# Kernel optimization log

Hardware: AMD Instinct MI355X
Metric: run time of the kernel (lower is better)

## Reference

```python
import jax, jax.numpy as jnp
import numpy as np

B, T, D, H, O = 128, 512, 512, 1024, 256
FORGET_BIAS = 1.0


def setup_inputs() -> dict:
    key = jax.random.key(0)
    ks = jax.random.split(key, 4)
    inputs = jax.random.normal(ks[0], (B * T, D), dtype=jnp.float32)
    # padded sequence lengths; ensure max == T so the reshape to [B, T, D] is exact
    seq_lens = jax.random.randint(ks[1], (B,), T // 2, T + 1, dtype=jnp.int32).at[0].set(T)
    c_in = jnp.zeros((B, H), jnp.float32)
    h_in = jnp.zeros((B, H), jnp.float32)
    W_lstm = jax.random.normal(ks[2], (D + H, 4 * H), dtype=jnp.float32) * (1.0 / np.sqrt(D + H))
    b_lstm = jnp.zeros((4 * H,), jnp.float32)
    W_out = jax.random.normal(ks[3], (H, O), dtype=jnp.float32) * 0.01  # normc_initializer(0.01)-scale
    b_out = jnp.zeros((O,), jnp.float32)
    return {"inputs": inputs, "c_in": c_in, "h_in": h_in, "W_lstm": W_lstm,
            "b_lstm": b_lstm, "W_out": W_out, "b_out": b_out, "seq_lens": seq_lens}


def reference(inputs, c_in, h_in, W_lstm, b_lstm, W_out, b_out, seq_lens):
    # add_time_dimension: [B*T, D] -> [B, T, D]; scan is time-major -> [T, B, D]
    xs = inputs.reshape(B, T, D).transpose(1, 0, 2)
    ts = jnp.arange(T, dtype=seq_lens.dtype)

    def step(carry, inp):
        c, h = carry
        x_t, t = inp
        gates = jnp.concatenate([x_t, h], axis=-1) @ W_lstm + b_lstm  # [B, 4H]
        i, j, f, o = jnp.split(gates, 4, axis=-1)  # BasicLSTMCell gate order
        new_c = c * jax.nn.sigmoid(f + FORGET_BIAS) + jax.nn.sigmoid(i) * jnp.tanh(j)
        new_h = jnp.tanh(new_c) * jax.nn.sigmoid(o)
        valid = (t < seq_lens)[:, None]  # dynamic_rnn sequence_length semantics
        c2 = jnp.where(valid, new_c, c)
        h2 = jnp.where(valid, new_h, h)
        out = jnp.where(valid, new_h, 0.0)  # outputs zeroed past seq_len
        return (c2, h2), out

    (c_out, h_out), outs = jax.lax.scan(step, (c_in, h_in), (xs, ts))
    lstm_out = outs.transpose(1, 0, 2).reshape(-1, H)  # [B*T, H]
    logits = lstm_out @ W_out + b_out  # [B*T, O]
    return logits, lstm_out, c_out, h_out
```

## Files before the change

### kernel.cpp

```cpp
#include <hip/hip_runtime.h>


typedef _Float16 f16;
typedef _Float16 half8 __attribute__((ext_vector_type(8)));
typedef float floatx4 __attribute__((ext_vector_type(4)));

#define AS1 __attribute__((address_space(1)))
#define AS3 __attribute__((address_space(3)))

__device__ __forceinline__ void gload_lds16(const void* g, void* l) {
  __builtin_amdgcn_global_load_lds((const AS1 void*)g, (AS3 void*)l, 16, 0, 0);
}
__device__ __forceinline__ void gload_lds16_coh(const void* g, void* l) {
  __builtin_amdgcn_global_load_lds((const AS1 void*)g, (AS3 void*)l, 16, 0, 17);
}

__device__ __forceinline__ int load_flag_coh(const int* p) {
  int v;
  asm volatile("global_load_dword %0, %1, off sc0 sc1\n\ts_waitcnt vmcnt(0)"
               : "=v"(v) : "v"(p) : "memory");
  return v;
}
__device__ __forceinline__ void store_flag_coh(int* p, int v) {
  asm volatile("global_store_dword %0, %1, off sc0 sc1" :: "v"(p), "v"(v) : "memory");
}
__device__ __forceinline__ void store_h_coh(f16* p, f16 v) {
  unsigned int uv = (unsigned int)__builtin_bit_cast(unsigned short, v);
  asm volatile("global_store_short %0, %1, off sc0 sc1" :: "v"(p), "v"(uv) : "memory");
}

__device__ __forceinline__ float sigm(float x) { return 1.f / (1.f + __expf(-x)); }
__device__ __forceinline__ float tanh_fast(float x) {
  float ax = fabsf(x);
  float e = __expf(2.f * ax);
  float t = 1.f - 2.f / (e + 1.f);
  return copysignf(t, x);
}

static constexpr size_t XW_OFF  = 0;
static constexpr size_t XW_BY   = (size_t)65536 * 4096 * 2;
static constexpr size_t L16_OFF = XW_OFF + XW_BY;
static constexpr size_t L16_BY  = (size_t)65536 * 1024 * 2;
static constexpr size_t IN16_OFF = L16_OFF;
static constexpr size_t WXT_OFF = L16_OFF + L16_BY;
static constexpr size_t WXT_BY  = (size_t)4096 * 512 * 2;
static constexpr size_t WOT_OFF = WXT_OFF + WXT_BY;
static constexpr size_t WOT_BY  = (size_t)256 * 1024 * 2;
static constexpr size_t WPK_OFF = WOT_OFF + WOT_BY;
static constexpr size_t WPK_BY  = (size_t)524288 * 8 * 2;
static constexpr size_t TH_OFF  = WPK_OFF + WPK_BY;
static constexpr size_t TH_BY   = (size_t)2 * 128 * 1024 * 2;
static constexpr size_t FLG_OFF = TH_OFF + TH_BY;
static constexpr size_t FLG_BY  = (size_t)8 * 32 * 4;
static constexpr size_t WS_NEED = FLG_OFF + FLG_BY;

__global__ __launch_bounds__(256) void conv_f32_to_f16(const float* __restrict__ in,
                                                       f16* __restrict__ out) {
  size_t i = (size_t)blockIdx.x * 256 + threadIdx.x;
  const float4* in4 = (const float4*)in;
  float4 a = in4[i * 2], b = in4[i * 2 + 1];
  half8 v = {(f16)a.x, (f16)a.y, (f16)a.z, (f16)a.w,
             (f16)b.x, (f16)b.y, (f16)b.z, (f16)b.w};
  *(half8*)(out + i * 8) = v;
}

__global__ __launch_bounds__(256) void transpose_f32_to_f16(const float* __restrict__ in,
                                                            f16* __restrict__ out,
                                                            int R, int C) {
  __shared__ float tile[64][65];
  int tx = threadIdx.x & 63, ty = threadIdx.x >> 6;
  int c0 = blockIdx.x * 64, r0 = blockIdx.y * 64;
#pragma unroll
  for (int q = 0; q < 16; ++q) {
    int r = q * 4 + ty;
    tile[r][tx] = in[(size_t)(r0 + r) * C + c0 + tx];
  }
  __syncthreads();
#pragma unroll
  for (int q = 0; q < 16; ++q) {
    int oc = q * 4 + ty;
    out[(size_t)(c0 + oc) * R + r0 + tx] = (f16)tile[tx][oc];
  }
}

__global__ __launch_bounds__(256) void pack_wh(const float* __restrict__ W,
                                               f16* __restrict__ wpack) {
  int s = blockIdx.x * 256 + threadIdx.x;
  int lane = s & 63;
  int ks = (s >> 6) & 7;
  int ni = (s >> 9) & 3;
  int w  = (s >> 11) & 7;
  int cb = s >> 14;
  int nh = w & 1, ksl = w >> 1;
  int c = nh * 64 + ni * 16 + (lane & 15);
  int g = c >> 5, ul = c & 31;
  int ncol = g * 1024 + cb * 32 + ul;
  int kb = ksl * 256 + ks * 32 + (lane >> 4) * 8;
  half8 v;
#pragma unroll
  for (int e = 0; e < 8; ++e)
    v[e] = (f16)W[(size_t)(512 + kb + e) * 4096 + ncol];
  ((half8*)wpack)[s] = v;
}

template <typename OT>
__global__ __launch_bounds__(256) void gemm_f16(const f16* __restrict__ A,
                                                const f16* __restrict__ Bt,
                                                const float* __restrict__ bias,
                                                OT* __restrict__ C,
                                                int M, int N, int K) {
  __shared__ __align__(16) char smem[32768];
  const int tid = threadIdx.x;
  const int n0 = blockIdx.x * 128, m0 = blockIdx.y * 128;
  const int l = tid & 63, w = tid >> 6;
  const int wr = w >> 1, wc = w & 1;
  const int r16 = l & 15, hi = l >> 4;
  floatx4 acc[4][4];
#pragma unroll
  for (int a = 0; a < 4; ++a)
#pragma unroll
    for (int b = 0; b < 4; ++b) acc[a][b] = (floatx4){0.f, 0.f, 0.f, 0.f};

  const int nk = K >> 6;
  for (int kk = 0; kk < nk; ++kk) {
    __syncthreads();
#pragma unroll
    for (int q = 0; q < 4; ++q) {
      int c = q * 256 + tid;
      int row = c >> 3, g8 = c & 7;
      gload_lds16(A + (size_t)(m0 + row) * K + kk * 64 + g8 * 8, smem + c * 16);
    }
#pragma unroll
    for (int q = 0; q < 4; ++q) {
      int c = q * 256 + tid;
      int row = c >> 3, g8 = c & 7;
      gload_lds16(Bt + (size_t)(n0 + row) * K + kk * 64 + g8 * 8, smem + 16384 + c * 16);
    }
    __syncthreads();
#pragma unroll
    for (int ks = 0; ks < 2; ++ks) {
      half8 af[4], bf[4];
#pragma unroll
      for (int mi = 0; mi < 4; ++mi)
        af[mi] = *(const half8*)(smem + ((wr * 64 + mi * 16 + r16) * 64 + ks * 32 + hi * 8) * 2);
#pragma unroll
      for (int ni = 0; ni < 4; ++ni)
        bf[ni] = *(const half8*)(smem + 16384 +
                                 ((wc * 64 + ni * 16 + r16) * 64 + ks * 32 + hi * 8) * 2);
#pragma unroll
      for (int mi = 0; mi < 4; ++mi)
#pragma unroll
        for (int ni = 0; ni < 4; ++ni)
          acc[mi][ni] = __builtin_amdgcn_mfma_f32_16x16x32_f16(af[mi], bf[ni], acc[mi][ni], 0, 0, 0);
    }
  }
#pragma unroll
  for (int ni = 0; ni < 4; ++ni) {
    int col = n0 + wc * 64 + ni * 16 + r16;
    float bv = bias[col];
#pragma unroll
    for (int mi = 0; mi < 4; ++mi)
#pragma unroll
      for (int rr = 0; rr < 4; ++rr) {
        int row = m0 + wr * 64 + mi * 16 + hi * 4 + rr;
        C[(size_t)row * N + col] = (OT)(acc[mi][ni][rr] + bv);
      }
  }
}

__global__ __launch_bounds__(512, 2)
void lstm_phase2(const f16* __restrict__ wpack, const f16* __restrict__ xw,
                 const float* __restrict__ c_in, const float* __restrict__ h_in,
                 const int* __restrict__ seq_lens,
                 f16* teamh, int* flags,
                 float* __restrict__ lstm_out, f16* __restrict__ lstm16,
                 float* __restrict__ c_out, float* __restrict__ h_out) {
  __shared__ __align__(16) char smem[65536];
  const int tid = threadIdx.x;
  const int bk = blockIdx.x;
  const int team = bk >> 5, cb = bk & 31;
  const int b0 = team * 16;
  const int u0 = cb * 32;
  const int l = tid & 63, w = tid >> 6;
  const int nh = w & 1, ksl = w >> 1;
  const int r16 = l & 15, hi = l >> 4;

  half8 wf[4][8];
  {
    const half8* wp = (const half8*)wpack;
    size_t base = (size_t)((cb * 8 + w) * 4) * 8 * 64;
#pragma unroll
    for (int ni = 0; ni < 4; ++ni)
#pragma unroll
      for (int ks = 0; ks < 8; ++ks)
        wf[ni][ks] = wp[base + (size_t)(ni * 8 + ks) * 64 + l];
  }

  const int bb = tid >> 5, ul = tid & 31;
  const int bglob = b0 + bb;
  const int nunit = u0 + ul;
  float creg = c_in[bglob * 1024 + nunit];
  float hreg = h_in[bglob * 1024 + nunit];
  const int slen = seq_lens[bglob];

  float* red = (float*)(smem + 32768);
  int* myflags = flags + team * 32;

#pragma unroll 1
  for (int t = 0; t < 512; ++t) {
    f16 xwv0, xwv1, xwv2, xwv3;
    {
      const f16* xp = xw + ((size_t)bglob * 512 + t) * 4096 + nunit;
      xwv0 = xp[0]; xwv1 = xp[1024]; xwv2 = xp[2048]; xwv3 = xp[3072];
    }

    if (t > 0) {
      if (tid < 64) {
        const int* fp = myflags + (tid & 31);
        while (true) {
          int g = load_flag_coh(fp);
          if (__all((tid >= 32) | (g >= t))) break;
          __builtin_amdgcn_s_sleep(1);
        }
      }
      __syncthreads();
      const char* hb = (const char*)teamh + (size_t)(t & 1) * (128 * 1024 * 2);
#pragma unroll
      for (int q = 0; q < 4; ++q) {
        int G = q * 512 + tid;
        int r = G >> 7, p = G & 127;
        int dg = p ^ (r & 7);
        gload_lds16_coh(hb + ((size_t)(b0 + r) * 1024 + dg * 8) * 2, smem + G * 16);
      }
    } else {
#pragma unroll
      for (int q = 0; q < 4; ++q) {
        int G = q * 512 + tid;
        int r = G >> 7, p = G & 127;
        int dg = p ^ (r & 7);
        const float* s = h_in + (size_t)(b0 + r) * 1024 + dg * 8;
        half8 v;
#pragma unroll
        for (int e = 0; e < 8; ++e) v[e] = (f16)s[e];
        *(half8*)(smem + G * 16) = v;
      }
    }
    __syncthreads();

    floatx4 acc0 = {0.f, 0.f, 0.f, 0.f}, acc1 = acc0, acc2 = acc0, acc3 = acc0;
#pragma unroll
    for (int ks = 0; ks < 8; ++ks) {
      int gran = ksl * 32 + ks * 4 + hi;
      int phys = gran ^ (r16 & 7);
      half8 a = *(const half8*)(smem + r16 * 2048 + phys * 16);
      acc0 = __builtin_amdgcn_mfma_f32_16x16x32_f16(a, wf[0][ks], acc0, 0, 0, 0);
      acc1 = __builtin_amdgcn_mfma_f32_16x16x32_f16(a, wf[1][ks], acc1, 0, 0, 0);
      acc2 = __builtin_amdgcn_mfma_f32_16x16x32_f16(a, wf[2][ks], acc2, 0, 0, 0);
      acc3 = __builtin_amdgcn_mfma_f32_16x16x32_f16(a, wf[3][ks], acc3, 0, 0, 0);
    }
    {
      int cbase = nh * 64 + r16;
      int rbase = ksl * 16 + hi * 4;
#pragma unroll
      for (int rr = 0; rr < 4; ++rr) {
        float* rp = red + (size_t)(rbase + rr) * 128 + cbase;
        rp[0] = acc0[rr]; rp[16] = acc1[rr]; rp[32] = acc2[rr]; rp[48] = acc3[rr];
      }
    }
    __syncthreads();

    float g0 = (float)xwv0, g1 = (float)xwv1, g2 = (float)xwv2, g3 = (float)xwv3;
#pragma unroll
    for (int p = 0; p < 4; ++p) {
      const float* rp = red + ((size_t)p * 16 + bb) * 128 + ul;
      g0 += rp[0]; g1 += rp[32]; g2 += rp[64]; g3 += rp[96];
    }
    float nc = creg * sigm(g2 + 1.f) + sigm(g0) * tanh_fast(g1);
    float nhv = tanh_fast(nc) * sigm(g3);
    bool valid = t < slen;
    if (valid) { creg = nc; hreg = nhv; }
    float outv = valid ? nhv : 0.f;
    size_t orow = ((size_t)bglob * 512 + t) * 1024 + nunit;

    store_h_coh(teamh + (size_t)((t + 1) & 1) * 131072 + bglob * 1024 + nunit, (f16)hreg);
    lstm_out[orow] = outv;
    lstm16[orow] = (f16)outv;

    asm volatile("s_waitcnt vmcnt(0)" ::: "memory");
    __syncthreads();
    if (tid == 0) store_flag_coh(myflags + cb, t + 1);
  }

  c_out[bglob * 1024 + nunit] = creg;
  h_out[bglob * 1024 + nunit] = hreg;
}

extern "C" void kernel_launch(void* const* d_in, const int* in_sizes, int n_in,
                              void* d_out, int out_size, void* d_ws, size_t ws_size,
                              hipStream_t stream) {
  const float* inputs  = (const float*)d_in[0];
  const float* c_in    = (const float*)d_in[1];
  const float* h_in    = (const float*)d_in[2];
  const float* W_lstm  = (const float*)d_in[3];
  const float* b_lstm  = (const float*)d_in[4];
  const float* W_out   = (const float*)d_in[5];
  const float* b_out   = (const float*)d_in[6];
  const int*   seq_lens= (const int*)d_in[7];

  float* logits  = (float*)d_out;
  float* lstm_out= logits + (size_t)65536 * 256;
  float* c_out   = lstm_out + (size_t)65536 * 1024;
  float* h_out   = c_out + (size_t)128 * 1024;

  if (ws_size < WS_NEED) return;

  char* ws = (char*)d_ws;
  f16* xw    = (f16*)(ws + XW_OFF);
  f16* in16  = (f16*)(ws + IN16_OFF);
  f16* l16   = (f16*)(ws + L16_OFF);
  f16* wxt   = (f16*)(ws + WXT_OFF);
  f16* wot   = (f16*)(ws + WOT_OFF);
  f16* wpk   = (f16*)(ws + WPK_OFF);
  f16* teamh = (f16*)(ws + TH_OFF);
  int* flags = (int*)(ws + FLG_OFF);

  hipMemsetAsync(flags, 0, FLG_BY, stream);
  conv_f32_to_f16<<<16384, 256, 0, stream>>>(inputs, in16);
  transpose_f32_to_f16<<<dim3(64, 8), 256, 0, stream>>>(W_lstm, wxt, 512, 4096);
  transpose_f32_to_f16<<<dim3(4, 16), 256, 0, stream>>>(W_out, wot, 1024, 256);
  pack_wh<<<2048, 256, 0, stream>>>(W_lstm, wpk);

  gemm_f16<f16><<<dim3(32, 512), 256, 0, stream>>>(in16, wxt, b_lstm, xw, 65536, 4096, 512);

  {
    const f16* wpk_c = wpk;
    const f16* xw_c  = xw;
    void* args[] = {(void*)&wpk_c, (void*)&xw_c, (void*)&c_in, (void*)&h_in,
                    (void*)&seq_lens, (void*)&teamh, (void*)&flags,
                    (void*)&lstm_out, (void*)&l16, (void*)&c_out, (void*)&h_out};
    hipLaunchCooperativeKernel((void*)lstm_phase2, dim3(256), dim3(512), args, 0, stream);
  }

  gemm_f16<float><<<dim3(2, 512), 256, 0, stream>>>(l16, wot, b_out, logits, 65536, 256, 1024);
}
```

Baseline: 2.379 ms.

## Replace per-block flag barrier with per-wave atomic counters and per-wave h loads

Each wave now atomically increments its block's step counter right after storing its h values. Consumer waves poll only the 8 producer blocks covering their K-slice and load just that slice of h directly into LDS. This removes the block-wide syncthreads and single-thread flag store from the critical step-to-step path. The LDS layout for h is reorganized per K-slice, and the reduction buffer gets an XOR swizzle to avoid bank conflicts. The costs are more atomic traffic and polling, plus subtler memory-ordering assumptions.

```diff
diff --git a/kernel.cpp b/kernel.cpp
--- a/kernel.cpp
+++ b/kernel.cpp
@@ -15,14 +15,11 @@
   __builtin_amdgcn_global_load_lds((const AS1 void*)g, (AS3 void*)l, 16, 0, 17);
 }
 
-__device__ __forceinline__ int load_flag_coh(const int* p) {
+__device__ __forceinline__ int load_flag_coh(const unsigned* p) {
   int v;
   asm volatile("global_load_dword %0, %1, off sc0 sc1\n\ts_waitcnt vmcnt(0)"
                : "=v"(v) : "v"(p) : "memory");
   return v;
-}
-__device__ __forceinline__ void store_flag_coh(int* p, int v) {
-  asm volatile("global_store_dword %0, %1, off sc0 sc1" :: "v"(p), "v"(v) : "memory");
 }
 __device__ __forceinline__ void store_h_coh(f16* p, f16 v) {
   unsigned int uv = (unsigned int)__builtin_bit_cast(unsigned short, v);
@@ -172,7 +169,7 @@
 void lstm_phase2(const f16* __restrict__ wpack, const f16* __restrict__ xw,
                  const float* __restrict__ c_in, const float* __restrict__ h_in,
                  const int* __restrict__ seq_lens,
-                 f16* teamh, int* flags,
+                 f16* teamh, unsigned* flags,
                  float* __restrict__ lstm_out, f16* __restrict__ lstm16,
                  float* __restrict__ c_out, float* __restrict__ h_out) {
   __shared__ __align__(16) char smem[65536];
@@ -204,7 +201,8 @@
   const int slen = seq_lens[bglob];
 
   float* red = (float*)(smem + 32768);
-  int* myflags = flags + team * 32;
+  unsigned* myflag = flags + team * 32 + cb;
+  const unsigned* pollf = flags + team * 32 + ksl * 8 + (l & 7);
 
 #pragma unroll 1
   for (int t = 0; t < 512; ++t) {
@@ -215,34 +213,33 @@
     }
 
     if (t > 0) {
-      if (tid < 64) {
-        const int* fp = myflags + (tid & 31);
-        while (true) {
-          int g = load_flag_coh(fp);
-          if (__all((tid >= 32) | (g >= t))) break;
-          __builtin_amdgcn_s_sleep(1);
-        }
-      }
-      __syncthreads();
-      const char* hb = (const char*)teamh + (size_t)(t & 1) * (128 * 1024 * 2);
-#pragma unroll
-      for (int q = 0; q < 4; ++q) {
-        int G = q * 512 + tid;
-        int r = G >> 7, p = G & 127;
-        int dg = p ^ (r & 7);
-        gload_lds16_coh(hb + ((size_t)(b0 + r) * 1024 + dg * 8) * 2, smem + G * 16);
-      }
+      const int tgt = 8 * t;
+      while (true) {
+        int g = load_flag_coh(pollf);
+        if (__all((l >= 8) || (g >= tgt))) break;
+        __builtin_amdgcn_s_sleep(1);
+      }
+      asm volatile("" ::: "memory");
+      const char* hb = (const char*)teamh + (size_t)(t & 1) * (131072 * 2);
+#pragma unroll
+      for (int j = 0; j < 4; ++j) {
+        int rj = nh * 8 + 2 * j + (l >> 5);
+        int ql = (l & 31) ^ (rj & 7);
+        gload_lds16_coh(hb + ((size_t)(b0 + rj) * 1024 + ksl * 256 + ql * 8) * 2,
+                        smem + (ksl * 512 + (nh * 8 + 2 * j) * 32) * 16);
+      }
+      asm volatile("s_waitcnt vmcnt(0)" ::: "memory");
     } else {
 #pragma unroll
-      for (int q = 0; q < 4; ++q) {
-        int G = q * 512 + tid;
-        int r = G >> 7, p = G & 127;
-        int dg = p ^ (r & 7);
-        const float* s = h_in + (size_t)(b0 + r) * 1024 + dg * 8;
+      for (int j = 0; j < 4; ++j) {
+        int idx = j * 512 + tid;
+        int ks_s = idx >> 9, rem = idx & 511, r = rem >> 5, qs = rem & 31;
+        int ql = qs ^ (r & 7);
+        const float* s = h_in + (size_t)(b0 + r) * 1024 + ks_s * 256 + ql * 8;
         half8 v;
 #pragma unroll
         for (int e = 0; e < 8; ++e) v[e] = (f16)s[e];
-        *(half8*)(smem + G * 16) = v;
+        *(half8*)(smem + idx * 16) = v;
       }
     }
     __syncthreads();
@@ -250,9 +247,8 @@
     floatx4 acc0 = {0.f, 0.f, 0.f, 0.f}, acc1 = acc0, acc2 = acc0, acc3 = acc0;
 #pragma unroll
     for (int ks = 0; ks < 8; ++ks) {
-      int gran = ksl * 32 + ks * 4 + hi;
-      int phys = gran ^ (r16 & 7);
-      half8 a = *(const half8*)(smem + r16 * 2048 + phys * 16);
+      int pq = (ks * 4 + hi) ^ (r16 & 7);
+      half8 a = *(const half8*)(smem + ksl * 8192 + r16 * 512 + pq * 16);
       acc0 = __builtin_amdgcn_mfma_f32_16x16x32_f16(a, wf[0][ks], acc0, 0, 0, 0);
       acc1 = __builtin_amdgcn_mfma_f32_16x16x32_f16(a, wf[1][ks], acc1, 0, 0, 0);
       acc2 = __builtin_amdgcn_mfma_f32_16x16x32_f16(a, wf[2][ks], acc2, 0, 0, 0);
@@ -263,8 +259,13 @@
       int rbase = ksl * 16 + hi * 4;
 #pragma unroll
       for (int rr = 0; rr < 4; ++rr) {
-        float* rp = red + (size_t)(rbase + rr) * 128 + cbase;
-        rp[0] = acc0[rr]; rp[16] = acc1[rr]; rp[32] = acc2[rr]; rp[48] = acc3[rr];
+        int rowr = rbase + rr;
+        unsigned sw = (unsigned)(rowr & 7) << 2;
+        float* rp = red + (size_t)rowr * 128;
+        rp[(cbase + 0) ^ sw]  = acc0[rr];
+        rp[(cbase + 16) ^ sw] = acc1[rr];
+        rp[(cbase + 32) ^ sw] = acc2[rr];
+        rp[(cbase + 48) ^ sw] = acc3[rr];
       }
     }
     __syncthreads();
@@ -272,8 +273,13 @@
     float g0 = (float)xwv0, g1 = (float)xwv1, g2 = (float)xwv2, g3 = (float)xwv3;
 #pragma unroll
     for (int p = 0; p < 4; ++p) {
-      const float* rp = red + ((size_t)p * 16 + bb) * 128 + ul;
-      g0 += rp[0]; g1 += rp[32]; g2 += rp[64]; g3 += rp[96];
+      int rowp = p * 16 + bb;
+      unsigned sw = (unsigned)(rowp & 7) << 2;
+      const float* rp = red + (size_t)rowp * 128;
+      g0 += rp[(ul + 0) ^ sw];
+      g1 += rp[(ul + 32) ^ sw];
+      g2 += rp[(ul + 64) ^ sw];
+      g3 += rp[(ul + 96) ^ sw];
     }
     float nc = creg * sigm(g2 + 1.f) + sigm(g0) * tanh_fast(g1);
     float nhv = tanh_fast(nc) * sigm(g3);
@@ -283,12 +289,11 @@
     size_t orow = ((size_t)bglob * 512 + t) * 1024 + nunit;
 
     store_h_coh(teamh + (size_t)((t + 1) & 1) * 131072 + bglob * 1024 + nunit, (f16)hreg);
+    asm volatile("s_waitcnt vmcnt(0)" ::: "memory");
+    if (l == 0)
+      __hip_atomic_fetch_add(myflag, 1u, __ATOMIC_RELAXED, __HIP_MEMORY_SCOPE_AGENT);
     lstm_out[orow] = outv;
     lstm16[orow] = (f16)outv;
-
-    asm volatile("s_waitcnt vmcnt(0)" ::: "memory");
-    __syncthreads();
-    if (tid == 0) store_flag_coh(myflags + cb, t + 1);
   }
 
   c_out[bglob * 1024 + nunit] = creg;
@@ -322,7 +327,7 @@
   f16* wot   = (f16*)(ws + WOT_OFF);
   f16* wpk   = (f16*)(ws + WPK_OFF);
   f16* teamh = (f16*)(ws + TH_OFF);
-  int* flags = (int*)(ws + FLG_OFF);
+  unsigned* flags = (unsigned*)(ws + FLG_OFF);
 
   hipMemsetAsync(flags, 0, FLG_BY, stream);
   conv_f32_to_f16<<<16384, 256, 0, stream>>>(inputs, in16);
```

After: 5.709 ms. 2.4x slower.

## Restructure LSTM recurrence: per-wave full-K weights, per-wave flags, drop LDS reduction

Applied to the files above, without the earlier changes.

Each wave now holds all 32 K-slices for 4 hidden units across the four gates, so every MFMA output lane holds a complete i/j/f/o set for one (batch, unit). This removes the cross-wave LDS reduction and one block barrier per step. Per-team h buffers and per-wave completion flags, polled with dwordx4 loads, replace the per-block flag and barrier before signalling. The xw prefetch now overlaps the flag spin on non-polling waves. In exchange the kernel holds 128 VGPRs of weights per lane and drops to one block per CU, and outputs are written from the rounded f16 h, which loses fp32 precision in lstm_out.

```diff
diff --git a/kernel.cpp b/kernel.cpp
--- a/kernel.cpp
+++ b/kernel.cpp
@@ -4,6 +4,7 @@
 typedef _Float16 f16;
 typedef _Float16 half8 __attribute__((ext_vector_type(8)));
 typedef float floatx4 __attribute__((ext_vector_type(4)));
+typedef unsigned u32x4 __attribute__((ext_vector_type(4)));
 
 #define AS1 __attribute__((address_space(1)))
 #define AS3 __attribute__((address_space(3)))
@@ -14,19 +15,18 @@
 __device__ __forceinline__ void gload_lds16_coh(const void* g, void* l) {
   __builtin_amdgcn_global_load_lds((const AS1 void*)g, (AS3 void*)l, 16, 0, 17);
 }
-
-__device__ __forceinline__ int load_flag_coh(const int* p) {
-  int v;
-  asm volatile("global_load_dword %0, %1, off sc0 sc1\n\ts_waitcnt vmcnt(0)"
+__device__ __forceinline__ void store_flag_coh(unsigned* p, unsigned v) {
+  asm volatile("global_store_dword %0, %1, off sc0 sc1" :: "v"(p), "v"(v) : "memory");
+}
+__device__ __forceinline__ void store_h_coh(f16* p, f16 v) {
+  unsigned uv = (unsigned)__builtin_bit_cast(unsigned short, v);
+  asm volatile("global_store_short %0, %1, off sc0 sc1" :: "v"(p), "v"(uv) : "memory");
+}
+__device__ __forceinline__ u32x4 load_flag4_coh(const unsigned* p) {
+  u32x4 v;
+  asm volatile("global_load_dwordx4 %0, %1, off sc0 sc1\n\ts_waitcnt vmcnt(0)"
                : "=v"(v) : "v"(p) : "memory");
   return v;
-}
-__device__ __forceinline__ void store_flag_coh(int* p, int v) {
-  asm volatile("global_store_dword %0, %1, off sc0 sc1" :: "v"(p), "v"(v) : "memory");
-}
-__device__ __forceinline__ void store_h_coh(f16* p, f16 v) {
-  unsigned int uv = (unsigned int)__builtin_bit_cast(unsigned short, v);
-  asm volatile("global_store_short %0, %1, off sc0 sc1" :: "v"(p), "v"(uv) : "memory");
 }
 
 __device__ __forceinline__ float sigm(float x) { return 1.f / (1.f + __expf(-x)); }
@@ -49,9 +49,9 @@
 static constexpr size_t WPK_OFF = WOT_OFF + WOT_BY;
 static constexpr size_t WPK_BY  = (size_t)524288 * 8 * 2;
 static constexpr size_t TH_OFF  = WPK_OFF + WPK_BY;
-static constexpr size_t TH_BY   = (size_t)2 * 128 * 1024 * 2;
+static constexpr size_t TH_BY   = (size_t)8 * 2 * 16 * 1024 * 2;
 static constexpr size_t FLG_OFF = TH_OFF + TH_BY;
-static constexpr size_t FLG_BY  = (size_t)8 * 32 * 4;
+static constexpr size_t FLG_BY  = (size_t)8 * 256 * 4;
 static constexpr size_t WS_NEED = FLG_OFF + FLG_BY;
 
 __global__ __launch_bounds__(256) void conv_f32_to_f16(const float* __restrict__ in,
@@ -87,15 +87,13 @@
                                                f16* __restrict__ wpack) {
   int s = blockIdx.x * 256 + threadIdx.x;
   int lane = s & 63;
-  int ks = (s >> 6) & 7;
-  int ni = (s >> 9) & 3;
-  int w  = (s >> 11) & 7;
+  int ks = (s >> 6) & 31;
+  int wv = (s >> 11) & 7;
   int cb = s >> 14;
-  int nh = w & 1, ksl = w >> 1;
-  int c = nh * 64 + ni * 16 + (lane & 15);
-  int g = c >> 5, ul = c & 31;
-  int ncol = g * 1024 + cb * 32 + ul;
-  int kb = ksl * 256 + ks * 32 + (lane >> 4) * 8;
+  int m = lane & 15;
+  int ul = m >> 2, g = m & 3;
+  int ncol = g * 1024 + cb * 32 + wv * 4 + ul;
+  int kb = ks * 32 + (lane >> 4) * 8;
   half8 v;
 #pragma unroll
   for (int e = 0; e < 8; ++e)
@@ -168,76 +166,77 @@
   }
 }
 
-__global__ __launch_bounds__(512, 2)
+__global__ __launch_bounds__(512, 1)
 void lstm_phase2(const f16* __restrict__ wpack, const f16* __restrict__ xw,
                  const float* __restrict__ c_in, const float* __restrict__ h_in,
                  const int* __restrict__ seq_lens,
-                 f16* teamh, int* flags,
+                 f16* teamh_all, unsigned* flags,
                  float* __restrict__ lstm_out, f16* __restrict__ lstm16,
                  float* __restrict__ c_out, float* __restrict__ h_out) {
-  __shared__ __align__(16) char smem[65536];
+  __shared__ __align__(16) char smem[34816];
   const int tid = threadIdx.x;
   const int bk = blockIdx.x;
   const int team = bk >> 5, cb = bk & 31;
   const int b0 = team * 16;
   const int u0 = cb * 32;
   const int l = tid & 63, w = tid >> 6;
-  const int nh = w & 1, ksl = w >> 1;
   const int r16 = l & 15, hi = l >> 4;
 
-  half8 wf[4][8];
+  half8 wf[32];
   {
     const half8* wp = (const half8*)wpack;
-    size_t base = (size_t)((cb * 8 + w) * 4) * 8 * 64;
-#pragma unroll
-    for (int ni = 0; ni < 4; ++ni)
-#pragma unroll
-      for (int ks = 0; ks < 8; ++ks)
-        wf[ni][ks] = wp[base + (size_t)(ni * 8 + ks) * 64 + l];
-  }
-
-  const int bb = tid >> 5, ul = tid & 31;
-  const int bglob = b0 + bb;
-  const int nunit = u0 + ul;
-  float creg = c_in[bglob * 1024 + nunit];
-  float hreg = h_in[bglob * 1024 + nunit];
-  const int slen = seq_lens[bglob];
-
-  float* red = (float*)(smem + 32768);
-  int* myflags = flags + team * 32;
+    size_t base = (size_t)(cb * 8 + w) * 32 * 64;
+#pragma unroll
+    for (int k = 0; k < 32; ++k) wf[k] = wp[base + (size_t)k * 64 + l];
+  }
+
+  const int bc = b0 + r16;
+  const int uloc = w * 4 + hi;
+  const int uc = u0 + uloc;
+  float creg = c_in[bc * 1024 + uc];
+  float hreg = h_in[bc * 1024 + uc];
+  const int slen_c = seq_lens[bc];
+  const f16* xwb = xw + ((size_t)bc * 512) * 4096 + uc;
+
+  const int b_r = tid >> 5, u_r = tid & 31;
+  const int slen_r = seq_lens[b0 + b_r];
+  f16* tile = (f16*)(smem + 32768);
+
+  f16* teamh = teamh_all + (size_t)team * 32768;
+  unsigned* tflags = flags + team * 256;
+  unsigned* wflag = tflags + cb * 8 + w;
+  const unsigned* pollp = tflags + l * 4;
 
 #pragma unroll 1
   for (int t = 0; t < 512; ++t) {
-    f16 xwv0, xwv1, xwv2, xwv3;
-    {
-      const f16* xp = xw + ((size_t)bglob * 512 + t) * 4096 + nunit;
-      xwv0 = xp[0]; xwv1 = xp[1024]; xwv2 = xp[2048]; xwv3 = xp[3072];
-    }
+    const int rb = t & 1, wb = rb ^ 1;
+    f16 xw0, xw1, xw2, xw3;
+    const f16* xp = xwb + (size_t)t * 4096;
 
     if (t > 0) {
-      if (tid < 64) {
-        const int* fp = myflags + (tid & 31);
+      if (w != 0) {
+        xw0 = xp[0]; xw1 = xp[1024]; xw2 = xp[2048]; xw3 = xp[3072];
+      } else {
         while (true) {
-          int g = load_flag_coh(fp);
-          if (__all((tid >= 32) | (g >= t))) break;
+          u32x4 v = load_flag4_coh(pollp);
+          bool ok = (int)v.x >= t && (int)v.y >= t && (int)v.z >= t && (int)v.w >= t;
+          if (__all(ok)) break;
           __builtin_amdgcn_s_sleep(1);
         }
       }
       __syncthreads();
-      const char* hb = (const char*)teamh + (size_t)(t & 1) * (128 * 1024 * 2);
+      const char* hb = (const char*)(teamh + (size_t)rb * 16384);
 #pragma unroll
       for (int q = 0; q < 4; ++q) {
-        int G = q * 512 + tid;
-        int r = G >> 7, p = G & 127;
-        int dg = p ^ (r & 7);
-        gload_lds16_coh(hb + ((size_t)(b0 + r) * 1024 + dg * 8) * 2, smem + G * 16);
+        int G = q * 512 + tid, r = G >> 7, p = G & 127, dg = p ^ (r & 7);
+        gload_lds16_coh(hb + (size_t)(r * 1024 + dg * 8) * 2, smem + G * 16);
       }
+      if (w == 0) { xw0 = xp[0]; xw1 = xp[1024]; xw2 = xp[2048]; xw3 = xp[3072]; }
     } else {
+      xw0 = xp[0]; xw1 = xp[1024]; xw2 = xp[2048]; xw3 = xp[3072];
 #pragma unroll
       for (int q = 0; q < 4; ++q) {
-        int G = q * 512 + tid;
-        int r = G >> 7, p = G & 127;
-        int dg = p ^ (r & 7);
+        int G = q * 512 + tid, r = G >> 7, p = G & 127, dg = p ^ (r & 7);
         const float* s = h_in + (size_t)(b0 + r) * 1024 + dg * 8;
         half8 v;
 #pragma unroll
@@ -247,52 +246,41 @@
     }
     __syncthreads();
 
-    floatx4 acc0 = {0.f, 0.f, 0.f, 0.f}, acc1 = acc0, acc2 = acc0, acc3 = acc0;
-#pragma unroll
-    for (int ks = 0; ks < 8; ++ks) {
-      int gran = ksl * 32 + ks * 4 + hi;
-      int phys = gran ^ (r16 & 7);
-      half8 a = *(const half8*)(smem + r16 * 2048 + phys * 16);
-      acc0 = __builtin_amdgcn_mfma_f32_16x16x32_f16(a, wf[0][ks], acc0, 0, 0, 0);
-      acc1 = __builtin_amdgcn_mfma_f32_16x16x32_f16(a, wf[1][ks], acc1, 0, 0, 0);
-      acc2 = __builtin_amdgcn_mfma_f32_16x16x32_f16(a, wf[2][ks], acc2, 0, 0, 0);
-      acc3 = __builtin_amdgcn_mfma_f32_16x16x32_f16(a, wf[3][ks], acc3, 0, 0, 0);
-    }
-    {
-      int cbase = nh * 64 + r16;
-      int rbase = ksl * 16 + hi * 4;
-#pragma unroll
-      for (int rr = 0; rr < 4; ++rr) {
-        float* rp = red + (size_t)(rbase + rr) * 128 + cbase;
-        rp[0] = acc0[rr]; rp[16] = acc1[rr]; rp[32] = acc2[rr]; rp[48] = acc3[rr];
-      }
-    }
+    floatx4 a0 = {0.f,0.f,0.f,0.f}, a1 = a0, a2 = a0, a3 = a0;
+    const int sw = l & 7;
+#pragma unroll
+    for (int k = 0; k < 8; ++k) {
+#define FR(K) (*(const half8*)(smem + r16 * 2048 + ((((K) * 4 + hi) ^ sw) * 16)))
+      a0 = __builtin_amdgcn_mfma_f32_16x16x32_f16(wf[k],      FR(k),      a0, 0, 0, 0);
+      a1 = __builtin_amdgcn_mfma_f32_16x16x32_f16(wf[8 + k],  FR(8 + k),  a1, 0, 0, 0);
+      a2 = __builtin_amdgcn_mfma_f32_16x16x32_f16(wf[16 + k], FR(16 + k), a2, 0, 0, 0);
+      a3 = __builtin_amdgcn_mfma_f32_16x16x32_f16(wf[24 + k], FR(24 + k), a3, 0, 0, 0);
+#undef FR
+    }
+    floatx4 sacc = (a0 + a1) + (a2 + a3);
+
+    float gi = sacc[0] + (float)xw0;
+    float gj = sacc[1] + (float)xw1;
+    float gf = sacc[2] + (float)xw2;
+    float go = sacc[3] + (float)xw3;
+    float nc = creg * sigm(gf + 1.f) + sigm(gi) * tanh_fast(gj);
+    float nhv = tanh_fast(nc) * sigm(go);
+    if (t < slen_c) { creg = nc; hreg = nhv; }
+    tile[r16 * 34 + uloc] = (f16)hreg;
     __syncthreads();
 
-    float g0 = (float)xwv0, g1 = (float)xwv1, g2 = (float)xwv2, g3 = (float)xwv3;
-#pragma unroll
-    for (int p = 0; p < 4; ++p) {
-      const float* rp = red + ((size_t)p * 16 + bb) * 128 + ul;
-      g0 += rp[0]; g1 += rp[32]; g2 += rp[64]; g3 += rp[96];
-    }
-    float nc = creg * sigm(g2 + 1.f) + sigm(g0) * tanh_fast(g1);
-    float nhv = tanh_fast(nc) * sigm(g3);
-    bool valid = t < slen;
-    if (valid) { creg = nc; hreg = nhv; }
-    float outv = valid ? nhv : 0.f;
-    size_t orow = ((size_t)bglob * 512 + t) * 1024 + nunit;
-
-    store_h_coh(teamh + (size_t)((t + 1) & 1) * 131072 + bglob * 1024 + nunit, (f16)hreg);
-    lstm_out[orow] = outv;
-    lstm16[orow] = (f16)outv;
-
+    f16 v16 = tile[b_r * 34 + u_r];
+    bool valid_r = t < slen_r;
+    size_t orow = ((size_t)(b0 + b_r) * 512 + t) * 1024 + u0 + u_r;
+    lstm_out[orow] = valid_r ? (float)v16 : 0.f;
+    lstm16[orow] = valid_r ? v16 : (f16)0;
+    store_h_coh(teamh + (size_t)wb * 16384 + b_r * 1024 + u0 + u_r, v16);
     asm volatile("s_waitcnt vmcnt(0)" ::: "memory");
-    __syncthreads();
-    if (tid == 0) store_flag_coh(myflags + cb, t + 1);
-  }
-
-  c_out[bglob * 1024 + nunit] = creg;
-  h_out[bglob * 1024 + nunit] = hreg;
+    if (l == 0) store_flag_coh(wflag, (unsigned)(t + 1));
+  }
+
+  c_out[bc * 1024 + uc] = creg;
+  h_out[bc * 1024 + uc] = hreg;
 }
 
 extern "C" void kernel_launch(void* const* d_in, const int* in_sizes, int n_in,
@@ -322,7 +310,7 @@
   f16* wot   = (f16*)(ws + WOT_OFF);
   f16* wpk   = (f16*)(ws + WPK_OFF);
   f16* teamh = (f16*)(ws + TH_OFF);
-  int* flags = (int*)(ws + FLG_OFF);
+  unsigned* flags = (unsigned*)(ws + FLG_OFF);
 
   hipMemsetAsync(flags, 0, FLG_BY, stream);
   conv_f32_to_f16<<<16384, 256, 0, stream>>>(inputs, in16);
```

New measurement: 3.479 ms. +46.3%, slower.
